# Optimization experiments

Hardware: AMD Instinct MI355X
Metric: run time of the kernel (lower is better)

Reference implementation:

```python
import jax, jax.numpy as jnp
import numpy as np

F = 32          # features
L2 = 16         # (max_degree+1)^2 spherical components, max_degree=3
K = 16          # num radial basis functions
CUTOFF = 6.0
GAMMA = 1.0
NZ = 119        # max_atomic_number + 1
KE = 14.399645  # Coulomb constant, eV*Angstrom
ZBL_C = np.array([0.18175, 0.50986, 0.28022, 0.02817], dtype=np.float32)
ZBL_D = np.array([3.19980, 0.94229, 0.40290, 0.20162], dtype=np.float32)


def _smooth_cutoff(r):
    u = jnp.minimum(r / CUTOFF, 1.0 - 1e-6)
    return jnp.where(r < CUTOFF, jnp.exp(-u * u / (1.0 - u * u)), 0.0)


def _radial(r):
    # exponential-Chebyshev radial basis: T_k(2*exp(-gamma*r)-1), k=0..K-1
    t = jnp.clip(2.0 * jnp.exp(-GAMMA * r) - 1.0, -1.0, 1.0)
    ks = jnp.arange(K, dtype=jnp.float32)
    return jnp.cos(ks[None, :] * jnp.arccos(t)[:, None])  # (E,K)


def _sph_harm(u):
    # real spherical harmonics up to l=3 on unit vectors u (E,3) -> (E,16)
    x, y, z = u[:, 0], u[:, 1], u[:, 2]
    x2, y2, z2 = x * x, y * y, z * z
    return jnp.stack([
        jnp.full_like(x, 0.282095),
        0.488603 * y, 0.488603 * z, 0.488603 * x,
        1.092548 * x * y, 1.092548 * y * z, 0.315392 * (3.0 * z2 - 1.0),
        1.092548 * x * z, 0.546274 * (x2 - y2),
        0.590044 * y * (3.0 * x2 - y2), 2.890611 * x * y * z,
        0.457046 * y * (5.0 * z2 - 1.0), 0.373176 * z * (5.0 * z2 - 3.0),
        0.457046 * x * (5.0 * z2 - 1.0), 1.445306 * z * (x2 - y2),
        0.590044 * x * (x2 - 3.0 * y2),
    ], axis=-1)


def setup_inputs() -> dict:
    key = jax.random.key(0)
    ks = jax.random.split(key, 16)
    N, E, B = 16384, 262144, 512
    atomic_numbers = jax.random.randint(ks[0], (N,), 0, 18)
    positions = jax.random.normal(ks[1], (N, 3), dtype=jnp.float32) * 3.0
    dst_idx = jax.random.randint(ks[2], (E,), 0, N)
    src_idx = jax.random.randint(ks[3], (E,), 0, N)
    batch_segments = jnp.sort(jax.random.randint(ks[4], (N,), 0, B))
    p = lambda k, shp, s: jax.random.normal(k, shp, dtype=jnp.float32) * s
    return {
        "atomic_numbers": atomic_numbers,
        "positions": positions,
        "dst_idx": dst_idx,
        "src_idx": src_idx,
        "batch_segments": batch_segments,
        "batch_size": B,
        "batch_mask": jnp.ones((B,), dtype=jnp.float32),
        "atom_mask": jnp.ones((N,), dtype=jnp.float32),
        "embed": p(ks[5], (NZ, F), 0.1),
        "Wr1_0": p(ks[6], (K, F), 0.25),
        "Wr2_0": p(ks[7], (K, F), 0.25),
        "W1_0": p(ks[8], (F, F), 0.18),
        "W2_0": p(ks[9], (F, F), 0.18),
        "Wr1_1": p(ks[10], (K, F), 0.25),
        "W1_1": p(ks[11], (F, F), 0.18),
        "W2_1": p(ks[12], (F, F), 0.18),
        "w_out": p(ks[13], (F,), 0.1),
        "b_out": p(ks[14], (NZ,), 0.1),
    }


def reference(atomic_numbers, positions, dst_idx, src_idx, batch_segments,
              batch_size, batch_mask, atom_mask, embed,
              Wr1_0, Wr2_0, W1_0, W2_0, Wr1_1, W1_1, W2_1, w_out, b_out):
    N = positions.shape[0]
    # ---- geometric features (gather on edges) ----
    disp = positions[src_idx] - positions[dst_idx]          # (E,3)
    r = jnp.sqrt(jnp.sum(disp * disp, axis=-1) + 1e-10)     # (E,)
    r = jnp.maximum(r, 1e-4)
    cut = _smooth_cutoff(r)                                  # (E,)
    rad = _radial(r) * cut[:, None]                          # (E,K)
    sh = _sph_harm(disp / r[:, None])                        # (E,L2)

    # ---- atom embedding lifted to equivariant features (N,L2,F) ----
    x = jnp.zeros((N, L2, F), dtype=jnp.float32).at[:, 0, :].set(embed[atomic_numbers])

    # ---- iteration 0: full-degree message passing ----
    g1 = rad @ Wr1_0                                         # (E,F) scalar->tensor path
    g2 = rad @ Wr2_0                                         # (E,F) degree-preserving path
    xs = x[src_idx]                                          # (E,L2,F)
    m = sh[:, :, None] * (g1[:, None, :] * xs[:, 0:1, :]) + g2[:, None, :] * xs
    x = jax.ops.segment_sum(m, dst_idx, num_segments=N)      # (N,L2,F)
    # refinement (equivariant gated residual MLP)
    h = jnp.einsum('nlf,fg->nlg', x, W1_0)
    x = x + jnp.einsum('nlf,fg->nlg', h * jax.nn.silu(h[:, 0:1, :]), W2_0)

    # ---- iteration 1: max_degree=0 message passing ----
    x0 = x[:, 0, :]                                          # (N,F)
    g = rad @ Wr1_1                                          # (E,F)
    x0 = jax.ops.segment_sum(g * x0[src_idx], dst_idx, num_segments=N)
    x0 = x0 + jax.nn.silu(x0 @ W1_1) @ W2_1                  # scalar refinement

    # ---- atomic energy readout ----
    e_atom = x0 @ w_out + b_out[atomic_numbers]              # (N,)

    # ---- ZBL nuclear repulsion over edges ----
    zf = atomic_numbers.astype(jnp.float32)
    zd, zs = zf[dst_idx], zf[src_idx]
    a = 0.8854 * 0.529177 / (zd ** 0.23 + zs ** 0.23 + 1e-10)
    phi = jnp.sum(ZBL_C[None, :] * jnp.exp(-ZBL_D[None, :] * (r / a)[:, None]), axis=-1)
    e_pair = 0.5 * KE * zd * zs / r * phi * cut
    e_atom = e_atom + jax.ops.segment_sum(e_pair, dst_idx, num_segments=N)

    e_atom = e_atom * atom_mask
    # scatter atomic energies to molecules
    e_mol = jax.ops.segment_sum(e_atom, batch_segments, num_segments=batch_size)
    return e_mol * batch_mask                                # (B,)
```

## Files before the change

kernel.cpp:

```cpp
#include <hip/hip_runtime.h>
#include <hip/hip_fp16.h>


#define FDIM 32
#define KDIM 16
#define BINCAP 32
#define MAXZ 18

__device__ __forceinline__ int pack_ct(float cut, float tt) {
    unsigned lo = __half_as_ushort(__float2half_rn(cut));
    unsigned hi = __half_as_ushort(__float2half_rn(tt));
    return (int)((hi << 16) | lo);
}
__device__ __forceinline__ float unpack_cut(int w) {
    return __half2float(__ushort_as_half((unsigned short)(w & 0xFFFF)));
}
__device__ __forceinline__ float unpack_tt(int w) {
    return __half2float(__ushort_as_half((unsigned short)(((unsigned)w) >> 16)));
}

__global__ __launch_bounds__(256) void edge_k(
    const int* __restrict__ dst, const int* __restrict__ src,
    const int* __restrict__ Z, const float* __restrict__ pos,
    int* __restrict__ counts, float* __restrict__ pair,
    int2* __restrict__ bins, int E)
{
    __shared__ float zpow[MAXZ];
    int tid = threadIdx.x;
    if (tid < MAXZ) zpow[tid] = __powf((float)tid, 0.23f);
    __syncthreads();

    int base = (blockIdx.x * 256 + tid) * 4;
    if (base >= E) return;
    int4 d4 = *(const int4*)(dst + base);
    int4 s4 = *(const int4*)(src + base);
    #pragma unroll
    for (int jj = 0; jj < 4; ++jj) {
        int d = (&d4.x)[jj], s = (&s4.x)[jj];
        float dx = pos[3 * s]     - pos[3 * d];
        float dy = pos[3 * s + 1] - pos[3 * d + 1];
        float dz = pos[3 * s + 2] - pos[3 * d + 2];
        float r2 = dx * dx + dy * dy + dz * dz;
        if (r2 >= 36.0f) continue;
        float r = fmaxf(sqrtf(r2 + 1e-10f), 1e-4f);
        float u = r * (1.0f / 6.0f);
        float u2 = u * u;
        float cut = __expf(-u2 / (1.0f - u2));
        float tt = fminf(fmaxf(2.0f * __expf(-r) - 1.0f, -1.0f), 1.0f);
        int zs_i = Z[s], zd_i = Z[d];
        float zd = (float)zd_i, zsf = (float)zs_i;
        float zsum = zpow[zd_i] + zpow[zs_i] + 1e-10f;
        float ra = r * zsum * (1.0f / 0.46853312f);
        float phi = 0.18175f * __expf(-3.1998f  * ra)
                  + 0.50986f * __expf(-0.94229f * ra)
                  + 0.28022f * __expf(-0.4029f  * ra)
                  + 0.02817f * __expf(-0.20162f * ra);
        atomicAdd(&pair[d], 0.5f * 14.399645f * zd * zsf / r * phi * cut);
        int slot = atomicAdd(&counts[d], 1);
        if (slot < BINCAP)
            bins[d * BINCAP + slot] = make_int2(s | (zs_i << 14), pack_ct(cut, tt));
    }
}

__global__ __launch_bounds__(256) void gather1_k(
    const int* __restrict__ counts, const int2* __restrict__ bins,
    const float* __restrict__ embed, const float* __restrict__ Wr1_0,
    const float* __restrict__ Wr2_0, const float* __restrict__ W1_0,
    const float* __restrict__ W2_0, float* __restrict__ x0, int N)
{
    __shared__ float Wc[KDIM * FDIM];
    __shared__ float W1s[FDIM * FDIM];
    __shared__ float W2s[FDIM * FDIM];
    __shared__ float emb_s[MAXZ * FDIM];
    int tid = threadIdx.x;
    for (int i = tid; i < KDIM * FDIM; i += 256)
        Wc[i] = 0.282095f * Wr1_0[i] + Wr2_0[i];
    for (int i = tid; i < FDIM * FDIM; i += 256) { W1s[i] = W1_0[i]; W2s[i] = W2_0[i]; }
    for (int i = tid; i < MAXZ * FDIM; i += 256) emb_s[i] = embed[i];
    __syncthreads();

    int w = (blockIdx.x * 256 + tid) >> 6;
    int lane = tid & 63, f = lane & 31;
    int a = 2 * w + (lane >> 5);
    if (a >= N) return;
    int deg = min(counts[a], BINCAP);
    int dm = max(__shfl(deg, 0), __shfl(deg, 32));
    const int2* row = bins + (size_t)a * BINCAP;
    float acc = 0.f;
    for (int i = 0; i < dm; i += 2) {
        int2 r0 = row[i];
        int2 r1 = row[i + 1];
        bool v0 = i < deg, v1 = (i + 1) < deg;
        float c0 = v0 ? unpack_cut(r0.y) : 0.f;
        float c1 = v1 ? unpack_cut(r1.y) : 0.f;
        int z0 = v0 ? ((r0.x >> 14) & 31) : 0;
        int z1 = v1 ? ((r1.x >> 14) & 31) : 0;
        float t0 = unpack_tt(r0.y), t1 = unpack_tt(r1.y);
        float A0 = 1.f, A1 = t0, B0 = 1.f, B1 = t1;
        float g0 = Wc[f] + Wc[FDIM + f] * t0;
        float g1 = Wc[f] + Wc[FDIM + f] * t1;
        #pragma unroll
        for (int k = 2; k < KDIM; ++k) {
            float A2 = 2.f * t0 * A1 - A0;
            float B2 = 2.f * t1 * B1 - B0;
            float wk = Wc[k * FDIM + f];
            g0 = fmaf(wk, A2, g0);
            g1 = fmaf(wk, B2, g1);
            A0 = A1; A1 = A2; B0 = B1; B1 = B2;
        }
        acc = fmaf(c0 * g0, emb_s[z0 * FDIM + f], acc);
        acc = fmaf(c1 * g1, emb_s[z1 * FDIM + f], acc);
    }
    float h = 0.f;
    #pragma unroll
    for (int g = 0; g < FDIM; ++g)
        h = fmaf(__shfl(acc, g, 32), W1s[g * FDIM + f], h);
    float cc = h * h / (1.0f + __expf(-h));
    float xo = acc;
    #pragma unroll
    for (int g = 0; g < FDIM; ++g)
        xo = fmaf(__shfl(cc, g, 32), W2s[g * FDIM + f], xo);
    x0[(size_t)a * FDIM + f] = xo;
}

__global__ __launch_bounds__(256) void gather2_k(
    const int* __restrict__ counts, const int2* __restrict__ bins,
    const float* __restrict__ x0, const float* __restrict__ pair,
    const float* __restrict__ Wr1_1, const float* __restrict__ W1_1,
    const float* __restrict__ W2_1, const float* __restrict__ w_out,
    const float* __restrict__ b_out, const int* __restrict__ Z,
    const int* __restrict__ bseg, const float* __restrict__ bmask,
    const float* __restrict__ amask, float* __restrict__ out, int N)
{
    __shared__ float Wg[KDIM * FDIM];
    __shared__ float W1s[FDIM * FDIM];
    __shared__ float W2s[FDIM * FDIM];
    __shared__ float wo[FDIM];
    int tid = threadIdx.x;
    for (int i = tid; i < KDIM * FDIM; i += 256) Wg[i] = Wr1_1[i];
    for (int i = tid; i < FDIM * FDIM; i += 256) { W1s[i] = W1_1[i]; W2s[i] = W2_1[i]; }
    if (tid < FDIM) wo[tid] = w_out[tid];
    __syncthreads();

    int w = (blockIdx.x * 256 + tid) >> 6;
    int lane = tid & 63, f = lane & 31;
    int a = 2 * w + (lane >> 5);
    if (a >= N) return;
    int deg = min(counts[a], BINCAP);
    int dm = max(__shfl(deg, 0), __shfl(deg, 32));
    const int2* row = bins + (size_t)a * BINCAP;
    float acc = 0.f;
    for (int i = 0; i < dm; i += 2) {
        int2 r0 = row[i];
        int2 r1 = row[i + 1];
        bool v0 = i < deg, v1 = (i + 1) < deg;
        int s0 = v0 ? (r0.x & 0x3FFF) : 0;
        int s1 = v1 ? (r1.x & 0x3FFF) : 0;
        float xa = x0[(size_t)s0 * FDIM + f];
        float xb = x0[(size_t)s1 * FDIM + f];
        float c0 = v0 ? unpack_cut(r0.y) : 0.f;
        float c1 = v1 ? unpack_cut(r1.y) : 0.f;
        float t0 = unpack_tt(r0.y), t1 = unpack_tt(r1.y);
        float A0 = 1.f, A1 = t0, B0 = 1.f, B1 = t1;
        float g0 = Wg[f] + Wg[FDIM + f] * t0;
        float g1 = Wg[f] + Wg[FDIM + f] * t1;
        #pragma unroll
        for (int k = 2; k < KDIM; ++k) {
            float A2 = 2.f * t0 * A1 - A0;
            float B2 = 2.f * t1 * B1 - B0;
            float wk = Wg[k * FDIM + f];
            g0 = fmaf(wk, A2, g0);
            g1 = fmaf(wk, B2, g1);
            A0 = A1; A1 = A2; B0 = B1; B1 = B2;
        }
        acc = fmaf(c0 * g0, xa, acc);
        acc = fmaf(c1 * g1, xb, acc);
    }
    float h = 0.f;
    #pragma unroll
    for (int g = 0; g < FDIM; ++g)
        h = fmaf(__shfl(acc, g, 32), W1s[g * FDIM + f], h);
    float cc = h / (1.0f + __expf(-h));
    float xo = acc;
    #pragma unroll
    for (int g = 0; g < FDIM; ++g)
        xo = fmaf(__shfl(cc, g, 32), W2s[g * FDIM + f], xo);
    float ea = xo * wo[f];
    #pragma unroll
    for (int m = 16; m >= 1; m >>= 1) ea += __shfl_xor(ea, m, 32);
    if ((lane & 31) == 0) {
        float e_atom = ea + b_out[Z[a]] + pair[a];
        int b = bseg[a];
        atomicAdd(&out[b], e_atom * amask[a] * bmask[b]);
    }
}

extern "C" void kernel_launch(void* const* d_in, const int* in_sizes, int n_in,
                              void* d_out, int out_size, void* d_ws, size_t ws_size,
                              hipStream_t stream) {
    int N = in_sizes[0];
    int E = in_sizes[2];
    int B = in_sizes[6];

    const int*   Z      = (const int*)d_in[0];
    const float* pos    = (const float*)d_in[1];
    const int*   dst    = (const int*)d_in[2];
    const int*   src    = (const int*)d_in[3];
    const int*   bseg   = (const int*)d_in[4];
    const float* bmask  = (const float*)d_in[6];
    const float* amask  = (const float*)d_in[7];
    const float* embed  = (const float*)d_in[8];
    const float* Wr1_0  = (const float*)d_in[9];
    const float* Wr2_0  = (const float*)d_in[10];
    const float* W1_0   = (const float*)d_in[11];
    const float* W2_0   = (const float*)d_in[12];
    const float* Wr1_1  = (const float*)d_in[13];
    const float* W1_1   = (const float*)d_in[14];
    const float* W2_1   = (const float*)d_in[15];
    const float* w_out  = (const float*)d_in[16];
    const float* b_out  = (const float*)d_in[17];
    float* out = (float*)d_out;

    int2*  bins   = (int2*)d_ws;
    int*   counts = (int*)(bins + (size_t)N * BINCAP);
    float* pair   = (float*)(counts + N);
    float* x0     = pair + N;

    hipMemsetAsync(counts, 0, (size_t)2 * N * sizeof(int), stream);
    hipMemsetAsync(out, 0, (size_t)B * sizeof(float), stream);

    int eb = (E / 4 + 255) / 256;
    edge_k<<<eb, 256, 0, stream>>>(dst, src, Z, pos, counts, pair, bins, E);

    int gb = (N / 2 * 64 + 255) / 256;
    gather1_k<<<gb, 256, 0, stream>>>(counts, bins, embed, Wr1_0, Wr2_0,
                                      W1_0, W2_0, x0, N);
    gather2_k<<<gb, 256, 0, stream>>>(counts, bins, x0, pair, Wr1_1, W1_1, W2_1,
                                      w_out, b_out, Z, bseg, bmask, amask, out, N);
}
```

Measured before the change: 149.7 us.

## Unroll gather loops by four, use one edge per thread, fuse memsets

Both gather kernels now walk each atom's bins four entries per iteration with int4 loads, which exposes four independent Chebyshev recurrences and four neighbour loads per iteration so more latency can be hidden. The edge kernel now gives each thread one edge instead of four, which raises thread-level parallelism for the scattered position loads and the atomics. The two memset calls become a single small zeroing kernel, trading two runtime calls for one launch. The wider unroll raises register pressure and does more padded work when the degree is not a multiple of four.

```diff
diff --git a/kernel.cpp b/kernel.cpp
--- a/kernel.cpp
+++ b/kernel.cpp
@@ -17,6 +17,13 @@
 }
 __device__ __forceinline__ float unpack_tt(int w) {
     return __half2float(__ushort_as_half((unsigned short)(((unsigned)w) >> 16)));
+}
+
+__global__ __launch_bounds__(256) void zero_k(int* __restrict__ p, int n2,
+                                              float* __restrict__ o, int b) {
+    int i = blockIdx.x * 256 + threadIdx.x;
+    if (i < n2) p[i] = 0;
+    if (i < b) o[i] = 0.f;
 }
 
 __global__ __launch_bounds__(256) void edge_k(
@@ -30,36 +37,32 @@
     if (tid < MAXZ) zpow[tid] = __powf((float)tid, 0.23f);
     __syncthreads();
 
-    int base = (blockIdx.x * 256 + tid) * 4;
-    if (base >= E) return;
-    int4 d4 = *(const int4*)(dst + base);
-    int4 s4 = *(const int4*)(src + base);
-    #pragma unroll
-    for (int jj = 0; jj < 4; ++jj) {
-        int d = (&d4.x)[jj], s = (&s4.x)[jj];
-        float dx = pos[3 * s]     - pos[3 * d];
-        float dy = pos[3 * s + 1] - pos[3 * d + 1];
-        float dz = pos[3 * s + 2] - pos[3 * d + 2];
-        float r2 = dx * dx + dy * dy + dz * dz;
-        if (r2 >= 36.0f) continue;
-        float r = fmaxf(sqrtf(r2 + 1e-10f), 1e-4f);
-        float u = r * (1.0f / 6.0f);
-        float u2 = u * u;
-        float cut = __expf(-u2 / (1.0f - u2));
-        float tt = fminf(fmaxf(2.0f * __expf(-r) - 1.0f, -1.0f), 1.0f);
-        int zs_i = Z[s], zd_i = Z[d];
-        float zd = (float)zd_i, zsf = (float)zs_i;
-        float zsum = zpow[zd_i] + zpow[zs_i] + 1e-10f;
-        float ra = r * zsum * (1.0f / 0.46853312f);
-        float phi = 0.18175f * __expf(-3.1998f  * ra)
-                  + 0.50986f * __expf(-0.94229f * ra)
-                  + 0.28022f * __expf(-0.4029f  * ra)
-                  + 0.02817f * __expf(-0.20162f * ra);
-        atomicAdd(&pair[d], 0.5f * 14.399645f * zd * zsf / r * phi * cut);
-        int slot = atomicAdd(&counts[d], 1);
-        if (slot < BINCAP)
-            bins[d * BINCAP + slot] = make_int2(s | (zs_i << 14), pack_ct(cut, tt));
-    }
+    int i = blockIdx.x * 256 + tid;
+    if (i >= E) return;
+    int d = dst[i], s = src[i];
+    float ax = pos[3 * s], ay = pos[3 * s + 1], az = pos[3 * s + 2];
+    float bx = pos[3 * d], by = pos[3 * d + 1], bz = pos[3 * d + 2];
+    float dx = ax - bx, dy = ay - by, dz = az - bz;
+    float r2 = dx * dx + dy * dy + dz * dz;
+    if (r2 >= 36.0f) return;
+
+    int zs_i = Z[s], zd_i = Z[d];
+    float r = fmaxf(sqrtf(r2 + 1e-10f), 1e-4f);
+    float u = r * (1.0f / 6.0f);
+    float u2 = u * u;
+    float cut = __expf(-u2 / (1.0f - u2));
+    float tt = fminf(fmaxf(2.0f * __expf(-r) - 1.0f, -1.0f), 1.0f);
+    float zd = (float)zd_i, zsf = (float)zs_i;
+    float zsum = zpow[zd_i] + zpow[zs_i] + 1e-10f;
+    float ra = r * zsum * (1.0f / 0.46853312f);
+    float phi = 0.18175f * __expf(-3.1998f  * ra)
+              + 0.50986f * __expf(-0.94229f * ra)
+              + 0.28022f * __expf(-0.4029f  * ra)
+              + 0.02817f * __expf(-0.20162f * ra);
+    atomicAdd(&pair[d], 0.5f * 14.399645f * zd * zsf / r * phi * cut);
+    int slot = atomicAdd(&counts[d], 1);
+    if (slot < BINCAP)
+        bins[d * BINCAP + slot] = make_int2(s | (zs_i << 14), pack_ct(cut, tt));
 }
 
 __global__ __launch_bounds__(256) void gather1_k(
@@ -85,31 +88,46 @@
     if (a >= N) return;
     int deg = min(counts[a], BINCAP);
     int dm = max(__shfl(deg, 0), __shfl(deg, 32));
-    const int2* row = bins + (size_t)a * BINCAP;
+    const int4* rq = (const int4*)(bins + (size_t)a * BINCAP);
     float acc = 0.f;
-    for (int i = 0; i < dm; i += 2) {
-        int2 r0 = row[i];
-        int2 r1 = row[i + 1];
-        bool v0 = i < deg, v1 = (i + 1) < deg;
-        float c0 = v0 ? unpack_cut(r0.y) : 0.f;
-        float c1 = v1 ? unpack_cut(r1.y) : 0.f;
-        int z0 = v0 ? ((r0.x >> 14) & 31) : 0;
-        int z1 = v1 ? ((r1.x >> 14) & 31) : 0;
-        float t0 = unpack_tt(r0.y), t1 = unpack_tt(r1.y);
+    for (int i = 0; i < dm; i += 4) {
+        int4 ra = rq[i >> 1];
+        int4 rb = rq[(i >> 1) + 1];
+        bool v0 = i < deg, v1 = i + 1 < deg, v2 = i + 2 < deg, v3 = i + 3 < deg;
+        float c0 = v0 ? unpack_cut(ra.y) : 0.f;
+        float c1 = v1 ? unpack_cut(ra.w) : 0.f;
+        float c2 = v2 ? unpack_cut(rb.y) : 0.f;
+        float c3 = v3 ? unpack_cut(rb.w) : 0.f;
+        int z0 = (ra.x >> 14) & 31, z1 = (ra.z >> 14) & 31;
+        int z2 = (rb.x >> 14) & 31, z3 = (rb.z >> 14) & 31;
+        float e0 = emb_s[(v0 ? z0 : 0) * FDIM + f];
+        float e1 = emb_s[(v1 ? z1 : 0) * FDIM + f];
+        float e2 = emb_s[(v2 ? z2 : 0) * FDIM + f];
+        float e3 = emb_s[(v3 ? z3 : 0) * FDIM + f];
+        float t0 = unpack_tt(ra.y), t1 = unpack_tt(ra.w);
+        float t2 = unpack_tt(rb.y), t3 = unpack_tt(rb.w);
         float A0 = 1.f, A1 = t0, B0 = 1.f, B1 = t1;
+        float C0 = 1.f, C1 = t2, D0 = 1.f, D1 = t3;
         float g0 = Wc[f] + Wc[FDIM + f] * t0;
         float g1 = Wc[f] + Wc[FDIM + f] * t1;
+        float g2 = Wc[f] + Wc[FDIM + f] * t2;
+        float g3 = Wc[f] + Wc[FDIM + f] * t3;
         #pragma unroll
         for (int k = 2; k < KDIM; ++k) {
             float A2 = 2.f * t0 * A1 - A0;
             float B2 = 2.f * t1 * B1 - B0;
+            float C2 = 2.f * t2 * C1 - C0;
+            float D2 = 2.f * t3 * D1 - D0;
             float wk = Wc[k * FDIM + f];
-            g0 = fmaf(wk, A2, g0);
-            g1 = fmaf(wk, B2, g1);
+            g0 = fmaf(wk, A2, g0); g1 = fmaf(wk, B2, g1);
+            g2 = fmaf(wk, C2, g2); g3 = fmaf(wk, D2, g3);
             A0 = A1; A1 = A2; B0 = B1; B1 = B2;
+            C0 = C1; C1 = C2; D0 = D1; D1 = D2;
         }
-        acc = fmaf(c0 * g0, emb_s[z0 * FDIM + f], acc);
-        acc = fmaf(c1 * g1, emb_s[z1 * FDIM + f], acc);
+        acc = fmaf(c0 * g0, e0, acc);
+        acc = fmaf(c1 * g1, e1, acc);
+        acc = fmaf(c2 * g2, e2, acc);
+        acc = fmaf(c3 * g3, e3, acc);
     }
     float h = 0.f;
     #pragma unroll
@@ -148,33 +166,48 @@
     if (a >= N) return;
     int deg = min(counts[a], BINCAP);
     int dm = max(__shfl(deg, 0), __shfl(deg, 32));
-    const int2* row = bins + (size_t)a * BINCAP;
+    const int4* rq = (const int4*)(bins + (size_t)a * BINCAP);
     float acc = 0.f;
-    for (int i = 0; i < dm; i += 2) {
-        int2 r0 = row[i];
-        int2 r1 = row[i + 1];
-        bool v0 = i < deg, v1 = (i + 1) < deg;
-        int s0 = v0 ? (r0.x & 0x3FFF) : 0;
-        int s1 = v1 ? (r1.x & 0x3FFF) : 0;
+    for (int i = 0; i < dm; i += 4) {
+        int4 ra = rq[i >> 1];
+        int4 rb = rq[(i >> 1) + 1];
+        bool v0 = i < deg, v1 = i + 1 < deg, v2 = i + 2 < deg, v3 = i + 3 < deg;
+        int s0 = v0 ? (ra.x & 0x3FFF) : 0;
+        int s1 = v1 ? (ra.z & 0x3FFF) : 0;
+        int s2 = v2 ? (rb.x & 0x3FFF) : 0;
+        int s3 = v3 ? (rb.z & 0x3FFF) : 0;
         float xa = x0[(size_t)s0 * FDIM + f];
         float xb = x0[(size_t)s1 * FDIM + f];
-        float c0 = v0 ? unpack_cut(r0.y) : 0.f;
-        float c1 = v1 ? unpack_cut(r1.y) : 0.f;
-        float t0 = unpack_tt(r0.y), t1 = unpack_tt(r1.y);
+        float xc = x0[(size_t)s2 * FDIM + f];
+        float xd = x0[(size_t)s3 * FDIM + f];
+        float c0 = v0 ? unpack_cut(ra.y) : 0.f;
+        float c1 = v1 ? unpack_cut(ra.w) : 0.f;
+        float c2 = v2 ? unpack_cut(rb.y) : 0.f;
+        float c3 = v3 ? unpack_cut(rb.w) : 0.f;
+        float t0 = unpack_tt(ra.y), t1 = unpack_tt(ra.w);
+        float t2 = unpack_tt(rb.y), t3 = unpack_tt(rb.w);
         float A0 = 1.f, A1 = t0, B0 = 1.f, B1 = t1;
+        float C0 = 1.f, C1 = t2, D0 = 1.f, D1 = t3;
         float g0 = Wg[f] + Wg[FDIM + f] * t0;
         float g1 = Wg[f] + Wg[FDIM + f] * t1;
+        float g2 = Wg[f] + Wg[FDIM + f] * t2;
+        float g3 = Wg[f] + Wg[FDIM + f] * t3;
         #pragma unroll
         for (int k = 2; k < KDIM; ++k) {
             float A2 = 2.f * t0 * A1 - A0;
             float B2 = 2.f * t1 * B1 - B0;
+            float C2 = 2.f * t2 * C1 - C0;
+            float D2 = 2.f * t3 * D1 - D0;
             float wk = Wg[k * FDIM + f];
-            g0 = fmaf(wk, A2, g0);
-            g1 = fmaf(wk, B2, g1);
+            g0 = fmaf(wk, A2, g0); g1 = fmaf(wk, B2, g1);
+            g2 = fmaf(wk, C2, g2); g3 = fmaf(wk, D2, g3);
             A0 = A1; A1 = A2; B0 = B1; B1 = B2;
+            C0 = C1; C1 = C2; D0 = D1; D1 = D2;
         }
         acc = fmaf(c0 * g0, xa, acc);
         acc = fmaf(c1 * g1, xb, acc);
+        acc = fmaf(c2 * g2, xc, acc);
+        acc = fmaf(c3 * g3, xd, acc);
     }
     float h = 0.f;
     #pragma unroll
@@ -226,10 +259,10 @@
     float* pair   = (float*)(counts + N);
     float* x0     = pair + N;
 
-    hipMemsetAsync(counts, 0, (size_t)2 * N * sizeof(int), stream);
-    hipMemsetAsync(out, 0, (size_t)B * sizeof(float), stream);
-
-    int eb = (E / 4 + 255) / 256;
+    int zb = (2 * N + 255) / 256;
+    zero_k<<<zb, 256, 0, stream>>>(counts, 2 * N, out, B);
+
+    int eb = (E + 255) / 256;
     edge_k<<<eb, 256, 0, stream>>>(dst, src, Z, pos, counts, pair, bins, E);
 
     int gb = (N / 2 * 64 + 255) / 256;
```

After: 146.8 us, median of 2. Within noise of the previous version (-1.9%).
